# Kernel optimization log

Hardware: AMD Instinct MI355X
Metric: run time of the kernel (lower is better)

Reference implementation:

```python
import jax, jax.numpy as jnp
import numpy as np

N_NODES = 100000
N_EDGES = 1600000
IN_CH = 128
HID = 128   # 2 * out_channels
OUT = 64


def setup_inputs() -> dict:
    key = jax.random.key(0)
    ks = jax.random.split(key, 6)
    x = jax.random.normal(ks[0], (N_NODES, IN_CH), dtype=jnp.float32)
    edge_index = jax.random.randint(ks[1], (2, N_EDGES), 0, N_NODES, dtype=jnp.int64)
    # Glorot-ish scaled weights
    W1 = jax.random.normal(ks[2], (IN_CH, HID), dtype=jnp.float32) * (1.0 / np.sqrt(IN_CH))
    b1 = jnp.zeros((HID,), dtype=jnp.float32)
    Wmu = jax.random.normal(ks[3], (HID, OUT), dtype=jnp.float32) * (1.0 / np.sqrt(HID))
    bmu = jnp.zeros((OUT,), dtype=jnp.float32)
    Wlv = jax.random.normal(ks[4], (HID, OUT), dtype=jnp.float32) * (1.0 / np.sqrt(HID))
    blv = jnp.zeros((OUT,), dtype=jnp.float32)
    return {"x": x, "edge_index": edge_index, "W1": W1, "b1": b1,
            "Wmu": Wmu, "bmu": bmu, "Wlv": Wlv, "blv": blv}


def reference(x, edge_index, W1, b1, Wmu, bmu, Wlv, blv):
    n = x.shape[0]
    loops = jnp.arange(n, dtype=edge_index.dtype)
    src = jnp.concatenate([edge_index[0], loops])  # [E + N]
    dst = jnp.concatenate([edge_index[1], loops])
    # GCN symmetric normalization with self-loops (cached=True -> compute once, reuse)
    deg = jax.ops.segment_sum(jnp.ones_like(src, dtype=x.dtype), dst, num_segments=n)
    dinv = jnp.where(deg > 0, jax.lax.rsqrt(jnp.maximum(deg, 1.0)), 0.0)
    norm = (dinv[src] * dinv[dst])[:, None]  # [E+N, 1]

    def gcn(h, W, b):
        h = h @ W                              # dense transform first (smaller gather width)
        msg = h[src] * norm                    # gather + edge scaling
        return jax.ops.segment_sum(msg, dst, num_segments=n) + b

    h = jax.nn.relu(gcn(x, W1, b1))
    mu = gcn(h, Wmu, bmu)
    logvar = gcn(h, Wlv, blv)
    return (mu, logvar)
```

## Files before the change

### kernel.cpp

```cpp
#include <hip/hip_runtime.h>
#include <hip/hip_fp16.h>


using half8 = __attribute__((ext_vector_type(8))) _Float16;
using f32x4 = __attribute__((ext_vector_type(4))) float;
using f32x2 = __attribute__((ext_vector_type(2))) float;

__global__ void detect_kernel(const int* __restrict__ ei, int* __restrict__ mode) {
    int lane = threadIdx.x & 63;
    int any = 0;
    for (int k = lane; k < 1024; k += 64) any |= ei[2 * k + 1];
    unsigned long long b = __ballot(any != 0);
    if (threadIdx.x == 0) *mode = (b == 0ull) ? 1 : 0;
}

__global__ __launch_bounds__(256) void bucket_count_kernel(
    const int* __restrict__ ei, int E, int n, const int* __restrict__ mode,
    int* __restrict__ bcnt) {
    __shared__ int h[512];
    int t = threadIdx.x;
    for (int i = t; i < 512; i += 256) h[i] = 0;
    __syncthreads();
    int m = *mode;
    int e0 = blockIdx.x * 4096;
#pragma unroll
    for (int k = 0; k < 16; ++k) {
        int e = e0 + k * 256 + t;
        if (e < E) {
            int s = m ? ei[2 * e] : ei[e];
            int d = m ? ei[2 * (E + e)] : ei[E + e];
            if ((unsigned)d < (unsigned)n && (unsigned)s < (unsigned)n)
                atomicAdd(&h[d >> 8], 1);
        }
    }
    __syncthreads();
    int K = (n + 255) >> 8;
    for (int b = t; b < K; b += 256)
        if (h[b]) atomicAdd(&bcnt[b], h[b]);
}

__global__ __launch_bounds__(512) void bucket_scan_kernel(
    const int* __restrict__ bcnt, int* __restrict__ bbase,
    int* __restrict__ cur, int* __restrict__ row_ptr_n, int K) {
    __shared__ int wtot[8];
    int tid = threadIdx.x, lane = tid & 63, wv = tid >> 6;
    int v = (tid < K) ? bcnt[tid] : 0;
    int incl = v;
#pragma unroll
    for (int off = 1; off < 64; off <<= 1) {
        int t = __shfl_up(incl, off, 64);
        if (lane >= off) incl += t;
    }
    if (lane == 63) wtot[wv] = incl;
    __syncthreads();
    int wo = 0;
    for (int w = 0; w < wv; ++w) wo += wtot[w];
    int ex = wo + incl - v;
    if (tid < K) {
        bbase[tid] = ex;
        cur[tid] = ex;
    }
    if (tid == K - 1) {
        bbase[K] = ex + v;
        *row_ptr_n = ex + v;
    }
}

__global__ __launch_bounds__(256) void partition_kernel(
    const int* __restrict__ ei, int E, int n, const int* __restrict__ mode,
    int* __restrict__ cur, int2* __restrict__ pairs) {
    __shared__ int hist[512];
    __shared__ int base[512];
    int t = threadIdx.x;
    for (int i = t; i < 512; i += 256) hist[i] = 0;
    __syncthreads();
    int m = *mode;
    int e0 = blockIdx.x * 4096;
    int s_[16], d_[16], o_[16];
#pragma unroll
    for (int k = 0; k < 16; ++k) {
        int e = e0 + k * 256 + t;
        d_[k] = -1;
        if (e < E) {
            int s = m ? ei[2 * e] : ei[e];
            int d = m ? ei[2 * (E + e)] : ei[E + e];
            if ((unsigned)d < (unsigned)n && (unsigned)s < (unsigned)n) {
                s_[k] = s;
                d_[k] = d;
                o_[k] = atomicAdd(&hist[d >> 8], 1);
            }
        }
    }
    __syncthreads();
    int K = (n + 255) >> 8;
    for (int b = t; b < K; b += 256) {
        int h = hist[b];
        base[b] = h ? atomicAdd(&cur[b], h) : 0;
    }
    __syncthreads();
#pragma unroll
    for (int k = 0; k < 16; ++k) {
        if (d_[k] >= 0) {
            int b = d_[k] >> 8;
            pairs[(size_t)(base[b] + o_[k])] = make_int2(s_[k], d_[k]);
        }
    }
}

__global__ __launch_bounds__(256) void build_kernel(
    const int2* __restrict__ pairs, const int* __restrict__ bbase,
    int* __restrict__ row_ptr, float* __restrict__ dinv,
    int* __restrict__ csr_src, int n) {
    __shared__ int hist[256];
    __shared__ int wtot[4];
    int b = blockIdx.x;
    int lo = b << 8;
    int beg = bbase[b], end = bbase[b + 1];
    int tid = threadIdx.x, lane = tid & 63, wv = tid >> 6;
    hist[tid] = 0;
    __syncthreads();
    for (int i = beg + tid; i < end; i += 256)
        atomicAdd(&hist[pairs[i].y & 255], 1);
    __syncthreads();
    int v = hist[tid];
    int incl = v;
#pragma unroll
    for (int off = 1; off < 64; off <<= 1) {
        int t = __shfl_up(incl, off, 64);
        if (lane >= off) incl += t;
    }
    if (lane == 63) wtot[wv] = incl;
    __syncthreads();
    int wo = 0;
    for (int w = 0; w < wv; ++w) wo += wtot[w];
    int ex = wo + incl - v;
    int node = lo + tid;
    if (node < n) {
        row_ptr[node] = beg + ex;
        dinv[node] = rsqrtf((float)(v + 1));
    }
    __syncthreads();
    hist[tid] = ex;
    __syncthreads();
    for (int i = beg + tid; i < end; i += 256) {
        int2 p = pairs[i];
        int pos = atomicAdd(&hist[p.y & 255], 1);
        csr_src[beg + pos] = p.x;
    }
}

template <int MODE>
__global__ __launch_bounds__(256) void agg_row_kernel(
    const __half* __restrict__ T, const float* __restrict__ dinv,
    const int* __restrict__ row_ptr, const int* __restrict__ csr_src,
    const float* __restrict__ bias, void* __restrict__ outa,
    void* __restrict__ outb, int n) {
    int wave = (int)((blockIdx.x * blockDim.x + threadIdx.x) >> 6);
    int lane = threadIdx.x & 63;
    if (wave >= n) return;
    const __half2* x2 = (const __half2*)T;
    float di = dinv[wave];
    float2 xf = __half22float2(x2[((size_t)wave << 6) + lane]);
    float ax = 0.f, ay = 0.f;
    int e = row_ptr[wave], end = row_ptr[wave + 1];
    for (; e + 8 <= end; e += 8) {
        int s[8];
        float w[8];
        float2 u[8];
#pragma unroll
        for (int k = 0; k < 8; ++k)
            s[k] = __builtin_amdgcn_readfirstlane(csr_src[e + k]);
#pragma unroll
        for (int k = 0; k < 8; ++k) w[k] = dinv[s[k]];
#pragma unroll
        for (int k = 0; k < 8; ++k)
            u[k] = __half22float2(x2[((size_t)s[k] << 6) + lane]);
#pragma unroll
        for (int k = 0; k < 8; ++k) {
            ax += w[k] * u[k].x;
            ay += w[k] * u[k].y;
        }
    }
    for (; e < end; ++e) {
        int s = __builtin_amdgcn_readfirstlane(csr_src[e]);
        float w = dinv[s];
        float2 u = __half22float2(x2[((size_t)s << 6) + lane]);
        ax += w * u.x;
        ay += w * u.y;
    }
    float2 bv = *(const float2*)(bias + 2 * lane);
    float vx = di * (di * xf.x + ax) + bv.x;
    float vy = di * (di * xf.y + ay) + bv.y;
    if (MODE == 0) {
        vx = fmaxf(vx, 0.f);
        vy = fmaxf(vy, 0.f);
        __half2 hv = __floats2half2_rn(vx, vy);
        unsigned int bits;
        __builtin_memcpy(&bits, &hv, 4);
        unsigned int* o = (unsigned int*)outa;
        __builtin_nontemporal_store(bits, o + ((size_t)wave << 6) + lane);
    } else {
        float* o = (lane < 32) ? (float*)outa : (float*)outb;
        int cc = (2 * lane) & 63;
        f32x2 v = {vx, vy};
        __builtin_nontemporal_store(v, (f32x2*)(o + (size_t)wave * 64 + cc));
    }
}

__global__ void packw_kernel(const float* __restrict__ Wa,
                             const float* __restrict__ Wb,
                             __half* __restrict__ dst) {
    int t = blockIdx.x * 256 + threadIdx.x;
    int lane = t & 63;
    int fk = t >> 6;
    int kt = fk & 3, nt = fk >> 2;
    int k0 = kt * 32 + ((lane >> 4) << 3);
    int c = nt * 16 + (lane & 15);
    const float* W;
    int ldw, cc;
    if (Wb) {
        W = (c < 64) ? Wa : Wb;
        cc = c & 63;
        ldw = 64;
    } else {
        W = Wa;
        cc = c;
        ldw = 128;
    }
    __half tmp[8];
#pragma unroll
    for (int e = 0; e < 8; ++e)
        tmp[e] = __float2half(W[(size_t)(k0 + e) * ldw + cc]);
    *(float4*)(dst + (size_t)t * 8) = *(float4*)tmp;
}

__global__ void packb_kernel(const float* __restrict__ bmu,
                             const float* __restrict__ blv,
                             float* __restrict__ bcomb) {
    int i = threadIdx.x;
    bcomb[i] = (i < 64) ? bmu[i] : blv[i - 64];
}

template <typename AT>
__global__ __launch_bounds__(256) void gemm_pure_kernel(
    const AT* __restrict__ A, const __half* __restrict__ Wp,
    __half* __restrict__ outh, int n) {
    int lane = threadIdx.x & 63;
    int wv = threadIdx.x >> 6;
    int m0 = (blockIdx.x * 4 + wv) * 16;
    if (m0 >= n) return;
    int row_a = m0 + (lane & 15);
    if (row_a >= n) row_a = n - 1;
    half8 afr[4];
    if constexpr (sizeof(AT) == 4) {
        const float4* Arow = (const float4*)(A + (size_t)row_a * 128);
#pragma unroll
        for (int kt = 0; kt < 4; ++kt) {
            float4 lo = Arow[kt * 8 + ((lane >> 4) << 1)];
            float4 hi = Arow[kt * 8 + ((lane >> 4) << 1) + 1];
            half8 h;
            h[0] = (_Float16)lo.x; h[1] = (_Float16)lo.y;
            h[2] = (_Float16)lo.z; h[3] = (_Float16)lo.w;
            h[4] = (_Float16)hi.x; h[5] = (_Float16)hi.y;
            h[6] = (_Float16)hi.z; h[7] = (_Float16)hi.w;
            afr[kt] = h;
        }
    } else {
        const half8* Arow = (const half8*)(A + (size_t)row_a * 128);
#pragma unroll
        for (int kt = 0; kt < 4; ++kt) afr[kt] = Arow[kt * 4 + (lane >> 4)];
    }

    const half8* Wf = (const half8*)Wp;
    int colw = lane & 15;
    int rbase = m0 + ((lane >> 4) << 2);

#pragma unroll
    for (int nt = 0; nt < 8; ++nt) {
        f32x4 acc = {0.f, 0.f, 0.f, 0.f};
#pragma unroll
        for (int kt = 0; kt < 4; ++kt)
            acc = __builtin_amdgcn_mfma_f32_16x16x32_f16(
                afr[kt], Wf[(nt * 4 + kt) * 64 + lane], acc, 0, 0, 0);
        int c = nt * 16 + colw;
#pragma unroll
        for (int e = 0; e < 4; ++e) {
            int r = rbase + e;
            if (r < n) outh[(size_t)r * 128 + c] = __float2half(acc[e]);
        }
    }
}

extern "C" void kernel_launch(void* const* d_in, const int* in_sizes, int n_in,
                              void* d_out, int out_size, void* d_ws, size_t ws_size,
                              hipStream_t stream) {
    const float* x   = (const float*)d_in[0];
    const int*   ei  = (const int*)d_in[1];
    const float* W1  = (const float*)d_in[2];
    const float* b1  = (const float*)d_in[3];
    const float* Wmu = (const float*)d_in[4];
    const float* bmu = (const float*)d_in[5];
    const float* Wlv = (const float*)d_in[6];
    const float* blv = (const float*)d_in[7];
    float* out = (float*)d_out;

    const int n = in_sizes[0] / 128;
    const int E = in_sizes[1] / 2;
    const int K = (n + 255) >> 8;

    char* ws = (char*)d_ws;
    size_t off = 0;
    auto alloc = [&](size_t bytes) -> void* {
        void* p = ws + off;
        off += (bytes + 255) & ~(size_t)255;
        return p;
    };
    int*   mode    = (int*)alloc(256);
    int*   bcnt    = (int*)alloc((size_t)K * 4);
    int*   bbase   = (int*)alloc((size_t)(K + 1) * 4);
    int*   bcur    = (int*)alloc((size_t)K * 4);
    int*   row_ptr = (int*)alloc((size_t)(n + 1) * 4);
    float* dinv    = (float*)alloc((size_t)n * 4);
    int*   csr_src = (int*)alloc((size_t)E * 4);
    int2*  pairs   = (int2*)alloc((size_t)E * 8);
    __half* bufT   = (__half*)alloc((size_t)n * 128 * 2);
    __half* bufH   = (__half*)alloc((size_t)n * 128 * 2);
    __half* W1p    = (__half*)alloc(128 * 128 * 2);
    __half* W2p    = (__half*)alloc(128 * 128 * 2);
    float* bcomb   = (float*)alloc(128 * 4);

    hipMemsetAsync(bcnt, 0, (size_t)K * 4, stream);

    detect_kernel<<<1, 64, 0, stream>>>(ei, mode);

    int pb = (E + 4095) / 4096;
    bucket_count_kernel<<<pb, 256, 0, stream>>>(ei, E, n, mode, bcnt);
    bucket_scan_kernel<<<1, 512, 0, stream>>>(bcnt, bbase, bcur,
                                              row_ptr + n, K);
    partition_kernel<<<pb, 256, 0, stream>>>(ei, E, n, mode, bcur, pairs);
    build_kernel<<<K, 256, 0, stream>>>(pairs, bbase, row_ptr, dinv,
                                        csr_src, n);

    packw_kernel<<<8, 256, 0, stream>>>(W1, nullptr, W1p);
    packw_kernel<<<8, 256, 0, stream>>>(Wmu, Wlv, W2p);
    packb_kernel<<<1, 128, 0, stream>>>(bmu, blv, bcomb);

    int gb = (n + 63) / 64;
    int ab = (n + 3) / 4;

    gemm_pure_kernel<float><<<gb, 256, 0, stream>>>(x, W1p, bufT, n);
    agg_row_kernel<0><<<ab, 256, 0, stream>>>(bufT, dinv, row_ptr, csr_src,
                                              b1, bufH, nullptr, n);
    gemm_pure_kernel<__half><<<gb, 256, 0, stream>>>(bufH, W2p, bufT, n);
    agg_row_kernel<1><<<ab, 256, 0, stream>>>(bufT, dinv, row_ptr, csr_src,
                                              bcomb, out, out + (size_t)n * 64, n);
}
```

Measured before the change: 260.4 us.

## Split features into two 64-wide halves and pack edge pairs into 32-bit words

Edge pairs are packed into one 32-bit word (24-bit source plus low 8 bits of the destination), halving partition and build traffic. Feature matrices are stored as two separate 64-column half buffers. Each aggregation pass handles one half, with the two half-waves each taking alternate edges and combining through a lane shuffle. The GEMMs write and read the split layout. The aim is a smaller per-pass gather working set that fits cache better, at the cost of reading the CSR twice and launching more kernels. Packing sources into 24 bits assumes fewer than 16.7M nodes.

```diff
diff --git a/kernel.cpp b/kernel.cpp
--- a/kernel.cpp
+++ b/kernel.cpp
@@ -68,7 +68,7 @@
 
 __global__ __launch_bounds__(256) void partition_kernel(
     const int* __restrict__ ei, int E, int n, const int* __restrict__ mode,
-    int* __restrict__ cur, int2* __restrict__ pairs) {
+    int* __restrict__ cur, unsigned* __restrict__ pairs) {
     __shared__ int hist[512];
     __shared__ int base[512];
     int t = threadIdx.x;
@@ -102,13 +102,14 @@
     for (int k = 0; k < 16; ++k) {
         if (d_[k] >= 0) {
             int b = d_[k] >> 8;
-            pairs[(size_t)(base[b] + o_[k])] = make_int2(s_[k], d_[k]);
+            unsigned p = (unsigned)s_[k] | ((unsigned)(d_[k] & 255) << 24);
+            pairs[(size_t)(base[b] + o_[k])] = p;
         }
     }
 }
 
 __global__ __launch_bounds__(256) void build_kernel(
-    const int2* __restrict__ pairs, const int* __restrict__ bbase,
+    const unsigned* __restrict__ pairs, const int* __restrict__ bbase,
     int* __restrict__ row_ptr, float* __restrict__ dinv,
     int* __restrict__ csr_src, int n) {
     __shared__ int hist[256];
@@ -120,7 +121,7 @@
     hist[tid] = 0;
     __syncthreads();
     for (int i = beg + tid; i < end; i += 256)
-        atomicAdd(&hist[pairs[i].y & 255], 1);
+        atomicAdd(&hist[pairs[i] >> 24], 1);
     __syncthreads();
     int v = hist[tid];
     int incl = v;
@@ -143,67 +144,78 @@
     hist[tid] = ex;
     __syncthreads();
     for (int i = beg + tid; i < end; i += 256) {
-        int2 p = pairs[i];
-        int pos = atomicAdd(&hist[p.y & 255], 1);
-        csr_src[beg + pos] = p.x;
+        unsigned p = pairs[i];
+        int pos = atomicAdd(&hist[p >> 24], 1);
+        csr_src[beg + pos] = (int)(p & 0x00FFFFFFu);
     }
 }
 
 template <int MODE>
-__global__ __launch_bounds__(256) void agg_row_kernel(
-    const __half* __restrict__ T, const float* __restrict__ dinv,
+__global__ __launch_bounds__(256) void agg_half_kernel(
+    const __half* __restrict__ S, const float* __restrict__ dinv,
     const int* __restrict__ row_ptr, const int* __restrict__ csr_src,
-    const float* __restrict__ bias, void* __restrict__ outa,
-    void* __restrict__ outb, int n) {
+    const float* __restrict__ bias, void* __restrict__ outp, int n) {
     int wave = (int)((blockIdx.x * blockDim.x + threadIdx.x) >> 6);
     int lane = threadIdx.x & 63;
     if (wave >= n) return;
-    const __half2* x2 = (const __half2*)T;
+    int g = lane >> 5;
+    int c = lane & 31;
+    const __half2* x2 = (const __half2*)S;
     float di = dinv[wave];
-    float2 xf = __half22float2(x2[((size_t)wave << 6) + lane]);
+    float2 self = __half22float2(x2[(size_t)wave * 32 + c]);
     float ax = 0.f, ay = 0.f;
     int e = row_ptr[wave], end = row_ptr[wave + 1];
     for (; e + 8 <= end; e += 8) {
-        int s[8];
-        float w[8];
-        float2 u[8];
-#pragma unroll
-        for (int k = 0; k < 8; ++k)
-            s[k] = __builtin_amdgcn_readfirstlane(csr_src[e + k]);
-#pragma unroll
-        for (int k = 0; k < 8; ++k) w[k] = dinv[s[k]];
-#pragma unroll
-        for (int k = 0; k < 8; ++k)
-            u[k] = __half22float2(x2[((size_t)s[k] << 6) + lane]);
-#pragma unroll
-        for (int k = 0; k < 8; ++k) {
+        int s[4];
+        float w[4];
+        float2 u[4];
+#pragma unroll
+        for (int k = 0; k < 4; ++k)
+            s[k] = __builtin_nontemporal_load(csr_src + e + 2 * k + g);
+#pragma unroll
+        for (int k = 0; k < 4; ++k)
+            u[k] = __half22float2(x2[(size_t)s[k] * 32 + c]);
+#pragma unroll
+        for (int k = 0; k < 4; ++k) w[k] = dinv[s[k]];
+#pragma unroll
+        for (int k = 0; k < 4; ++k) {
             ax += w[k] * u[k].x;
             ay += w[k] * u[k].y;
         }
     }
-    for (; e < end; ++e) {
-        int s = __builtin_amdgcn_readfirstlane(csr_src[e]);
+    for (; e + 2 <= end; e += 2) {
+        int s = __builtin_nontemporal_load(csr_src + e + g);
         float w = dinv[s];
-        float2 u = __half22float2(x2[((size_t)s << 6) + lane]);
+        float2 u = __half22float2(x2[(size_t)s * 32 + c]);
         ax += w * u.x;
         ay += w * u.y;
     }
-    float2 bv = *(const float2*)(bias + 2 * lane);
-    float vx = di * (di * xf.x + ax) + bv.x;
-    float vy = di * (di * xf.y + ay) + bv.y;
-    if (MODE == 0) {
-        vx = fmaxf(vx, 0.f);
-        vy = fmaxf(vy, 0.f);
-        __half2 hv = __floats2half2_rn(vx, vy);
-        unsigned int bits;
-        __builtin_memcpy(&bits, &hv, 4);
-        unsigned int* o = (unsigned int*)outa;
-        __builtin_nontemporal_store(bits, o + ((size_t)wave << 6) + lane);
-    } else {
-        float* o = (lane < 32) ? (float*)outa : (float*)outb;
-        int cc = (2 * lane) & 63;
-        f32x2 v = {vx, vy};
-        __builtin_nontemporal_store(v, (f32x2*)(o + (size_t)wave * 64 + cc));
+    if (e < end) {
+        int s = __builtin_nontemporal_load(csr_src + e);
+        float w = g ? 0.f : dinv[s];
+        float2 u = __half22float2(x2[(size_t)s * 32 + c]);
+        ax += w * u.x;
+        ay += w * u.y;
+    }
+    ax += __shfl_xor(ax, 32);
+    ay += __shfl_xor(ay, 32);
+    if (lane < 32) {
+        float2 bv = *(const float2*)(bias + 2 * c);
+        float vx = di * (di * self.x + ax) + bv.x;
+        float vy = di * (di * self.y + ay) + bv.y;
+        if (MODE == 0) {
+            vx = fmaxf(vx, 0.f);
+            vy = fmaxf(vy, 0.f);
+            __half2 hv = __floats2half2_rn(vx, vy);
+            unsigned int bits;
+            __builtin_memcpy(&bits, &hv, 4);
+            unsigned int* o = (unsigned int*)outp;
+            __builtin_nontemporal_store(bits, o + (size_t)wave * 32 + c);
+        } else {
+            f32x2 v = {vx, vy};
+            float* o = (float*)outp;
+            __builtin_nontemporal_store(v, (f32x2*)(o + (size_t)wave * 64 + 2 * c));
+        }
     }
 }
 
@@ -234,17 +246,9 @@
     *(float4*)(dst + (size_t)t * 8) = *(float4*)tmp;
 }
 
-__global__ void packb_kernel(const float* __restrict__ bmu,
-                             const float* __restrict__ blv,
-                             float* __restrict__ bcomb) {
-    int i = threadIdx.x;
-    bcomb[i] = (i < 64) ? bmu[i] : blv[i - 64];
-}
-
-template <typename AT>
-__global__ __launch_bounds__(256) void gemm_pure_kernel(
-    const AT* __restrict__ A, const __half* __restrict__ Wp,
-    __half* __restrict__ outh, int n) {
+__global__ __launch_bounds__(256) void gemm_f32_kernel(
+    const float* __restrict__ A, const __half* __restrict__ Wp,
+    __half* __restrict__ o0, __half* __restrict__ o1, int n) {
     int lane = threadIdx.x & 63;
     int wv = threadIdx.x >> 6;
     int m0 = (blockIdx.x * 4 + wv) * 16;
@@ -252,29 +256,21 @@
     int row_a = m0 + (lane & 15);
     if (row_a >= n) row_a = n - 1;
     half8 afr[4];
-    if constexpr (sizeof(AT) == 4) {
-        const float4* Arow = (const float4*)(A + (size_t)row_a * 128);
-#pragma unroll
-        for (int kt = 0; kt < 4; ++kt) {
-            float4 lo = Arow[kt * 8 + ((lane >> 4) << 1)];
-            float4 hi = Arow[kt * 8 + ((lane >> 4) << 1) + 1];
-            half8 h;
-            h[0] = (_Float16)lo.x; h[1] = (_Float16)lo.y;
-            h[2] = (_Float16)lo.z; h[3] = (_Float16)lo.w;
-            h[4] = (_Float16)hi.x; h[5] = (_Float16)hi.y;
-            h[6] = (_Float16)hi.z; h[7] = (_Float16)hi.w;
-            afr[kt] = h;
-        }
-    } else {
-        const half8* Arow = (const half8*)(A + (size_t)row_a * 128);
-#pragma unroll
-        for (int kt = 0; kt < 4; ++kt) afr[kt] = Arow[kt * 4 + (lane >> 4)];
-    }
-
+    const float4* Arow = (const float4*)(A + (size_t)row_a * 128);
+#pragma unroll
+    for (int kt = 0; kt < 4; ++kt) {
+        float4 lo = Arow[kt * 8 + ((lane >> 4) << 1)];
+        float4 hi = Arow[kt * 8 + ((lane >> 4) << 1) + 1];
+        half8 h;
+        h[0] = (_Float16)lo.x; h[1] = (_Float16)lo.y;
+        h[2] = (_Float16)lo.z; h[3] = (_Float16)lo.w;
+        h[4] = (_Float16)hi.x; h[5] = (_Float16)hi.y;
+        h[6] = (_Float16)hi.z; h[7] = (_Float16)hi.w;
+        afr[kt] = h;
+    }
     const half8* Wf = (const half8*)Wp;
     int colw = lane & 15;
     int rbase = m0 + ((lane >> 4) << 2);
-
 #pragma unroll
     for (int nt = 0; nt < 8; ++nt) {
         f32x4 acc = {0.f, 0.f, 0.f, 0.f};
@@ -282,11 +278,49 @@
         for (int kt = 0; kt < 4; ++kt)
             acc = __builtin_amdgcn_mfma_f32_16x16x32_f16(
                 afr[kt], Wf[(nt * 4 + kt) * 64 + lane], acc, 0, 0, 0);
-        int c = nt * 16 + colw;
+        __half* o = (nt < 4) ? o0 : o1;
+        int c = (nt & 3) * 16 + colw;
 #pragma unroll
         for (int e = 0; e < 4; ++e) {
             int r = rbase + e;
-            if (r < n) outh[(size_t)r * 128 + c] = __float2half(acc[e]);
+            if (r < n) o[(size_t)r * 64 + c] = __float2half(acc[e]);
+        }
+    }
+}
+
+__global__ __launch_bounds__(256) void gemm_h16_kernel(
+    const __half* __restrict__ A0, const __half* __restrict__ A1,
+    const __half* __restrict__ Wp,
+    __half* __restrict__ o0, __half* __restrict__ o1, int n) {
+    int lane = threadIdx.x & 63;
+    int wv = threadIdx.x >> 6;
+    int m0 = (blockIdx.x * 4 + wv) * 16;
+    if (m0 >= n) return;
+    int row_a = m0 + (lane & 15);
+    if (row_a >= n) row_a = n - 1;
+    half8 afr[4];
+#pragma unroll
+    for (int kt = 0; kt < 4; ++kt) {
+        const __half* Ap = (kt < 2) ? A0 : A1;
+        int cc = (kt & 1) * 32 + ((lane >> 4) << 3);
+        afr[kt] = *(const half8*)(Ap + (size_t)row_a * 64 + cc);
+    }
+    const half8* Wf = (const half8*)Wp;
+    int colw = lane & 15;
+    int rbase = m0 + ((lane >> 4) << 2);
+#pragma unroll
+    for (int nt = 0; nt < 8; ++nt) {
+        f32x4 acc = {0.f, 0.f, 0.f, 0.f};
+#pragma unroll
+        for (int kt = 0; kt < 4; ++kt)
+            acc = __builtin_amdgcn_mfma_f32_16x16x32_f16(
+                afr[kt], Wf[(nt * 4 + kt) * 64 + lane], acc, 0, 0, 0);
+        __half* o = (nt < 4) ? o0 : o1;
+        int c = (nt & 3) * 16 + colw;
+#pragma unroll
+        for (int e = 0; e < 4; ++e) {
+            int r = rbase + e;
+            if (r < n) o[(size_t)r * 64 + c] = __float2half(acc[e]);
         }
     }
 }
@@ -315,19 +349,20 @@
         off += (bytes + 255) & ~(size_t)255;
         return p;
     };
-    int*   mode    = (int*)alloc(256);
-    int*   bcnt    = (int*)alloc((size_t)K * 4);
-    int*   bbase   = (int*)alloc((size_t)(K + 1) * 4);
-    int*   bcur    = (int*)alloc((size_t)K * 4);
-    int*   row_ptr = (int*)alloc((size_t)(n + 1) * 4);
-    float* dinv    = (float*)alloc((size_t)n * 4);
-    int*   csr_src = (int*)alloc((size_t)E * 4);
-    int2*  pairs   = (int2*)alloc((size_t)E * 8);
-    __half* bufT   = (__half*)alloc((size_t)n * 128 * 2);
-    __half* bufH   = (__half*)alloc((size_t)n * 128 * 2);
-    __half* W1p    = (__half*)alloc(128 * 128 * 2);
-    __half* W2p    = (__half*)alloc(128 * 128 * 2);
-    float* bcomb   = (float*)alloc(128 * 4);
+    int*      mode    = (int*)alloc(256);
+    int*      bcnt    = (int*)alloc((size_t)K * 4);
+    int*      bbase   = (int*)alloc((size_t)(K + 1) * 4);
+    int*      bcur    = (int*)alloc((size_t)K * 4);
+    int*      row_ptr = (int*)alloc((size_t)(n + 1) * 4);
+    float*    dinv    = (float*)alloc((size_t)n * 4);
+    int*      csr_src = (int*)alloc((size_t)E * 4);
+    unsigned* pairs   = (unsigned*)alloc((size_t)E * 4);
+    __half*   T0      = (__half*)alloc((size_t)n * 64 * 2);
+    __half*   T1      = (__half*)alloc((size_t)n * 64 * 2);
+    __half*   H0      = (__half*)alloc((size_t)n * 64 * 2);
+    __half*   H1      = (__half*)alloc((size_t)n * 64 * 2);
+    __half*   W1p     = (__half*)alloc(128 * 128 * 2);
+    __half*   W2p     = (__half*)alloc(128 * 128 * 2);
 
     hipMemsetAsync(bcnt, 0, (size_t)K * 4, stream);
 
@@ -343,15 +378,18 @@
 
     packw_kernel<<<8, 256, 0, stream>>>(W1, nullptr, W1p);
     packw_kernel<<<8, 256, 0, stream>>>(Wmu, Wlv, W2p);
-    packb_kernel<<<1, 128, 0, stream>>>(bmu, blv, bcomb);
 
     int gb = (n + 63) / 64;
     int ab = (n + 3) / 4;
 
-    gemm_pure_kernel<float><<<gb, 256, 0, stream>>>(x, W1p, bufT, n);
-    agg_row_kernel<0><<<ab, 256, 0, stream>>>(bufT, dinv, row_ptr, csr_src,
-                                              b1, bufH, nullptr, n);
-    gemm_pure_kernel<__half><<<gb, 256, 0, stream>>>(bufH, W2p, bufT, n);
-    agg_row_kernel<1><<<ab, 256, 0, stream>>>(bufT, dinv, row_ptr, csr_src,
-                                              bcomb, out, out + (size_t)n * 64, n);
-}
+    gemm_f32_kernel<<<gb, 256, 0, stream>>>(x, W1p, T0, T1, n);
+    agg_half_kernel<0><<<ab, 256, 0, stream>>>(T0, dinv, row_ptr, csr_src,
+                                               b1, H0, n);
+    agg_half_kernel<0><<<ab, 256, 0, stream>>>(T1, dinv, row_ptr, csr_src,
+                                               b1 + 64, H1, n);
+    gemm_h16_kernel<<<gb, 256, 0, stream>>>(H0, H1, W2p, T0, T1, n);
+    agg_half_kernel<1><<<ab, 256, 0, stream>>>(T0, dinv, row_ptr, csr_src,
+                                               bmu, out, n);
+    agg_half_kernel<1><<<ab, 256, 0, stream>>>(T1, dinv, row_ptr, csr_src,
+                                               blv, out + (size_t)n * 64, n);
+}
```

Result: slower. 364.0 us (+39.8%).

## Replace count-scan edge partition with fixed-capacity buckets and packed pairs

Applied to the files above, without the earlier changes.

Removes the bucket-count and bucket-scan kernels by giving each 256-node bucket a fixed slot range of CAP entries, so the partition kernel takes offsets directly from atomic bucket counters. Edge pairs are packed into 32 bits (24-bit source plus the 8-bit local destination), halving pair traffic. Row ranges are stored as int2 begin/end pairs, and the bias-packing kernel is replaced by selecting the bias pointer per lane. This saves one full pass over edge_index and two launches, but it assumes no bucket holds more than CAP edges and that node ids fit in 24 bits, and it enlarges the workspace.

```diff
diff --git a/kernel.cpp b/kernel.cpp
--- a/kernel.cpp
+++ b/kernel.cpp
@@ -5,6 +5,8 @@
 using half8 = __attribute__((ext_vector_type(8))) _Float16;
 using f32x4 = __attribute__((ext_vector_type(4))) float;
 using f32x2 = __attribute__((ext_vector_type(2))) float;
+
+constexpr int CAP = 8192;
 
 __global__ void detect_kernel(const int* __restrict__ ei, int* __restrict__ mode) {
     int lane = threadIdx.x & 63;
@@ -14,61 +16,9 @@
     if (threadIdx.x == 0) *mode = (b == 0ull) ? 1 : 0;
 }
 
-__global__ __launch_bounds__(256) void bucket_count_kernel(
-    const int* __restrict__ ei, int E, int n, const int* __restrict__ mode,
-    int* __restrict__ bcnt) {
-    __shared__ int h[512];
-    int t = threadIdx.x;
-    for (int i = t; i < 512; i += 256) h[i] = 0;
-    __syncthreads();
-    int m = *mode;
-    int e0 = blockIdx.x * 4096;
-#pragma unroll
-    for (int k = 0; k < 16; ++k) {
-        int e = e0 + k * 256 + t;
-        if (e < E) {
-            int s = m ? ei[2 * e] : ei[e];
-            int d = m ? ei[2 * (E + e)] : ei[E + e];
-            if ((unsigned)d < (unsigned)n && (unsigned)s < (unsigned)n)
-                atomicAdd(&h[d >> 8], 1);
-        }
-    }
-    __syncthreads();
-    int K = (n + 255) >> 8;
-    for (int b = t; b < K; b += 256)
-        if (h[b]) atomicAdd(&bcnt[b], h[b]);
-}
-
-__global__ __launch_bounds__(512) void bucket_scan_kernel(
-    const int* __restrict__ bcnt, int* __restrict__ bbase,
-    int* __restrict__ cur, int* __restrict__ row_ptr_n, int K) {
-    __shared__ int wtot[8];
-    int tid = threadIdx.x, lane = tid & 63, wv = tid >> 6;
-    int v = (tid < K) ? bcnt[tid] : 0;
-    int incl = v;
-#pragma unroll
-    for (int off = 1; off < 64; off <<= 1) {
-        int t = __shfl_up(incl, off, 64);
-        if (lane >= off) incl += t;
-    }
-    if (lane == 63) wtot[wv] = incl;
-    __syncthreads();
-    int wo = 0;
-    for (int w = 0; w < wv; ++w) wo += wtot[w];
-    int ex = wo + incl - v;
-    if (tid < K) {
-        bbase[tid] = ex;
-        cur[tid] = ex;
-    }
-    if (tid == K - 1) {
-        bbase[K] = ex + v;
-        *row_ptr_n = ex + v;
-    }
-}
-
 __global__ __launch_bounds__(256) void partition_kernel(
     const int* __restrict__ ei, int E, int n, const int* __restrict__ mode,
-    int* __restrict__ cur, int2* __restrict__ pairs) {
+    int* __restrict__ bcnt, unsigned* __restrict__ pairs) {
     __shared__ int hist[512];
     __shared__ int base[512];
     int t = threadIdx.x;
@@ -95,32 +45,33 @@
     int K = (n + 255) >> 8;
     for (int b = t; b < K; b += 256) {
         int h = hist[b];
-        base[b] = h ? atomicAdd(&cur[b], h) : 0;
+        base[b] = h ? atomicAdd(&bcnt[b], h) : 0;
     }
     __syncthreads();
 #pragma unroll
     for (int k = 0; k < 16; ++k) {
         if (d_[k] >= 0) {
             int b = d_[k] >> 8;
-            pairs[(size_t)(base[b] + o_[k])] = make_int2(s_[k], d_[k]);
+            unsigned p = (unsigned)s_[k] | ((unsigned)(d_[k] & 255) << 24);
+            pairs[(size_t)b * CAP + base[b] + o_[k]] = p;
         }
     }
 }
 
 __global__ __launch_bounds__(256) void build_kernel(
-    const int2* __restrict__ pairs, const int* __restrict__ bbase,
-    int* __restrict__ row_ptr, float* __restrict__ dinv,
+    const unsigned* __restrict__ pairs, const int* __restrict__ bcnt,
+    int2* __restrict__ rowbe, float* __restrict__ dinv,
     int* __restrict__ csr_src, int n) {
     __shared__ int hist[256];
     __shared__ int wtot[4];
     int b = blockIdx.x;
-    int lo = b << 8;
-    int beg = bbase[b], end = bbase[b + 1];
+    int cnt = bcnt[b];
+    size_t gbase = (size_t)b * CAP;
     int tid = threadIdx.x, lane = tid & 63, wv = tid >> 6;
     hist[tid] = 0;
     __syncthreads();
-    for (int i = beg + tid; i < end; i += 256)
-        atomicAdd(&hist[pairs[i].y & 255], 1);
+    for (int i = tid; i < cnt; i += 256)
+        atomicAdd(&hist[pairs[gbase + i] >> 24], 1);
     __syncthreads();
     int v = hist[tid];
     int incl = v;
@@ -134,27 +85,28 @@
     int wo = 0;
     for (int w = 0; w < wv; ++w) wo += wtot[w];
     int ex = wo + incl - v;
-    int node = lo + tid;
+    int node = (b << 8) + tid;
     if (node < n) {
-        row_ptr[node] = beg + ex;
+        int beg = (int)gbase + ex;
+        rowbe[node] = make_int2(beg, beg + v);
         dinv[node] = rsqrtf((float)(v + 1));
     }
     __syncthreads();
     hist[tid] = ex;
     __syncthreads();
-    for (int i = beg + tid; i < end; i += 256) {
-        int2 p = pairs[i];
-        int pos = atomicAdd(&hist[p.y & 255], 1);
-        csr_src[beg + pos] = p.x;
+    for (int i = tid; i < cnt; i += 256) {
+        unsigned p = pairs[gbase + i];
+        int pos = atomicAdd(&hist[p >> 24], 1);
+        csr_src[gbase + pos] = (int)(p & 0x00FFFFFFu);
     }
 }
 
 template <int MODE>
 __global__ __launch_bounds__(256) void agg_row_kernel(
     const __half* __restrict__ T, const float* __restrict__ dinv,
-    const int* __restrict__ row_ptr, const int* __restrict__ csr_src,
-    const float* __restrict__ bias, void* __restrict__ outa,
-    void* __restrict__ outb, int n) {
+    const int2* __restrict__ rowbe, const int* __restrict__ csr_src,
+    const float* __restrict__ biasa, const float* __restrict__ biasb,
+    void* __restrict__ outa, void* __restrict__ outb, int n) {
     int wave = (int)((blockIdx.x * blockDim.x + threadIdx.x) >> 6);
     int lane = threadIdx.x & 63;
     if (wave >= n) return;
@@ -162,7 +114,8 @@
     float di = dinv[wave];
     float2 xf = __half22float2(x2[((size_t)wave << 6) + lane]);
     float ax = 0.f, ay = 0.f;
-    int e = row_ptr[wave], end = row_ptr[wave + 1];
+    int2 be = rowbe[wave];
+    int e = be.x, end = be.y;
     for (; e + 8 <= end; e += 8) {
         int s[8];
         float w[8];
@@ -188,7 +141,8 @@
         ax += w * u.x;
         ay += w * u.y;
     }
-    float2 bv = *(const float2*)(bias + 2 * lane);
+    const float* bp = (lane < 32) ? biasa : biasb;
+    float2 bv = *(const float2*)(bp + ((2 * lane) & 63));
     float vx = di * (di * xf.x + ax) + bv.x;
     float vy = di * (di * xf.y + ay) + bv.y;
     if (MODE == 0) {
@@ -234,13 +188,6 @@
     *(float4*)(dst + (size_t)t * 8) = *(float4*)tmp;
 }
 
-__global__ void packb_kernel(const float* __restrict__ bmu,
-                             const float* __restrict__ blv,
-                             float* __restrict__ bcomb) {
-    int i = threadIdx.x;
-    bcomb[i] = (i < 64) ? bmu[i] : blv[i - 64];
-}
-
 template <typename AT>
 __global__ __launch_bounds__(256) void gemm_pure_kernel(
     const AT* __restrict__ A, const __half* __restrict__ Wp,
@@ -315,43 +262,36 @@
         off += (bytes + 255) & ~(size_t)255;
         return p;
     };
-    int*   mode    = (int*)alloc(256);
-    int*   bcnt    = (int*)alloc((size_t)K * 4);
-    int*   bbase   = (int*)alloc((size_t)(K + 1) * 4);
-    int*   bcur    = (int*)alloc((size_t)K * 4);
-    int*   row_ptr = (int*)alloc((size_t)(n + 1) * 4);
-    float* dinv    = (float*)alloc((size_t)n * 4);
-    int*   csr_src = (int*)alloc((size_t)E * 4);
-    int2*  pairs   = (int2*)alloc((size_t)E * 8);
-    __half* bufT   = (__half*)alloc((size_t)n * 128 * 2);
-    __half* bufH   = (__half*)alloc((size_t)n * 128 * 2);
-    __half* W1p    = (__half*)alloc(128 * 128 * 2);
-    __half* W2p    = (__half*)alloc(128 * 128 * 2);
-    float* bcomb   = (float*)alloc(128 * 4);
+    int*      mode    = (int*)alloc(256);
+    int*      bcnt    = (int*)alloc((size_t)K * 4);
+    int2*     rowbe   = (int2*)alloc((size_t)n * 8);
+    float*    dinv    = (float*)alloc((size_t)n * 4);
+    int*      csr_src = (int*)alloc((size_t)K * CAP * 4);
+    unsigned* pairs   = (unsigned*)alloc((size_t)K * CAP * 4);
+    __half*   bufT    = (__half*)alloc((size_t)n * 128 * 2);
+    __half*   bufH    = (__half*)alloc((size_t)n * 128 * 2);
+    __half*   W1p     = (__half*)alloc(128 * 128 * 2);
+    __half*   W2p     = (__half*)alloc(128 * 128 * 2);
 
     hipMemsetAsync(bcnt, 0, (size_t)K * 4, stream);
 
     detect_kernel<<<1, 64, 0, stream>>>(ei, mode);
 
     int pb = (E + 4095) / 4096;
-    bucket_count_kernel<<<pb, 256, 0, stream>>>(ei, E, n, mode, bcnt);
-    bucket_scan_kernel<<<1, 512, 0, stream>>>(bcnt, bbase, bcur,
-                                              row_ptr + n, K);
-    partition_kernel<<<pb, 256, 0, stream>>>(ei, E, n, mode, bcur, pairs);
-    build_kernel<<<K, 256, 0, stream>>>(pairs, bbase, row_ptr, dinv,
-                                        csr_src, n);
+    partition_kernel<<<pb, 256, 0, stream>>>(ei, E, n, mode, bcnt, pairs);
+    build_kernel<<<K, 256, 0, stream>>>(pairs, bcnt, rowbe, dinv, csr_src, n);
 
     packw_kernel<<<8, 256, 0, stream>>>(W1, nullptr, W1p);
     packw_kernel<<<8, 256, 0, stream>>>(Wmu, Wlv, W2p);
-    packb_kernel<<<1, 128, 0, stream>>>(bmu, blv, bcomb);
 
     int gb = (n + 63) / 64;
     int ab = (n + 3) / 4;
 
     gemm_pure_kernel<float><<<gb, 256, 0, stream>>>(x, W1p, bufT, n);
-    agg_row_kernel<0><<<ab, 256, 0, stream>>>(bufT, dinv, row_ptr, csr_src,
-                                              b1, bufH, nullptr, n);
+    agg_row_kernel<0><<<ab, 256, 0, stream>>>(bufT, dinv, rowbe, csr_src,
+                                              b1, b1 + 64, bufH, nullptr, n);
     gemm_pure_kernel<__half><<<gb, 256, 0, stream>>>(bufH, W2p, bufT, n);
-    agg_row_kernel<1><<<ab, 256, 0, stream>>>(bufT, dinv, row_ptr, csr_src,
-                                              bcomb, out, out + (size_t)n * 64, n);
-}
+    agg_row_kernel<1><<<ab, 256, 0, stream>>>(bufT, dinv, rowbe, csr_src,
+                                              bmu, blv, out,
+                                              out + (size_t)n * 64, n);
+}
```

Measured after the change: 244.2 us. 6.2% less time.
